# Kernel optimization log

Hardware: AMD Instinct MI355X
Metric: run time of the kernel (lower is better)

The kernel has to match this reference:

```python
import jax, jax.numpy as jnp
import numpy as np

HIDDEN = 2048
N_HEAD = 16
N_KV_HEAD = 4
HEAD_DIM = HIDDEN // N_HEAD
B, S = 2, 2048


def setup_inputs() -> dict:
    key = jax.random.key(0)
    ks = jax.random.split(key, 10)
    scale = 1.0 / np.sqrt(HIDDEN)
    x = jax.random.normal(ks[0], (B, S, HIDDEN), dtype=jnp.float32)
    # causal additive mask, broadcastable over batch and heads
    causal = jnp.tril(jnp.ones((S, S), dtype=jnp.bool_))
    attention_mask = jnp.where(causal, 0.0, -1e9).astype(jnp.float32)[None, None]
    wq_w = jax.random.uniform(ks[1], (HIDDEN, HIDDEN), jnp.float32, -scale, scale)
    wq_b = jax.random.uniform(ks[2], (HIDDEN,), jnp.float32, -scale, scale)
    wk_w = jax.random.uniform(ks[3], (N_KV_HEAD * HEAD_DIM, HIDDEN), jnp.float32, -scale, scale)
    wk_b = jax.random.uniform(ks[4], (N_KV_HEAD * HEAD_DIM,), jnp.float32, -scale, scale)
    wv_w = jax.random.uniform(ks[5], (N_KV_HEAD * HEAD_DIM, HIDDEN), jnp.float32, -scale, scale)
    wv_b = jax.random.uniform(ks[6], (N_KV_HEAD * HEAD_DIM,), jnp.float32, -scale, scale)
    wo_w = jax.random.uniform(ks[7], (HIDDEN, HIDDEN), jnp.float32, -scale, scale)
    wo_b = jax.random.uniform(ks[8], (HIDDEN,), jnp.float32, -scale, scale)
    return dict(x=x, attention_mask=attention_mask, wq_w=wq_w, wq_b=wq_b,
                wk_w=wk_w, wk_b=wk_b, wv_w=wv_w, wv_b=wv_b, wo_w=wo_w, wo_b=wo_b)


def reference(x, attention_mask, wq_w, wq_b, wk_w, wk_b, wv_w, wv_b, wo_w, wo_b):
    bs, seq_len, _ = x.shape
    group = N_HEAD // N_KV_HEAD
    q = x @ wq_w.T + wq_b  # [B,S,H*D]
    k = x @ wk_w.T + wk_b  # [B,S,Hkv*D]
    v = x @ wv_w.T + wv_b
    q = q.reshape(bs, seq_len, N_HEAD, HEAD_DIM).transpose(0, 2, 1, 3)        # [B,H,S,D]
    k = k.reshape(bs, seq_len, N_KV_HEAD, HEAD_DIM).transpose(0, 2, 1, 3)     # [B,Hkv,S,D]
    v = v.reshape(bs, seq_len, N_KV_HEAD, HEAD_DIM).transpose(0, 2, 1, 3)
    # GQA: share each kv head across `group` query heads (repeat_interleave equiv)
    qg = q.reshape(bs, N_KV_HEAD, group, seq_len, HEAD_DIM)
    scores = jnp.einsum('bkgqd,bkld->bkgql', qg, k) / np.sqrt(HEAD_DIM)       # [B,Hkv,g,S,S]
    scores = scores + attention_mask[:, :, None]  # mask broadcast over head dims
    attn = jax.nn.softmax(scores, axis=-1)  # dropout is identity at inference
    out = jnp.einsum('bkgql,bkld->bkgqd', attn, v)                             # [B,Hkv,g,S,D]
    out = out.reshape(bs, N_HEAD, seq_len, HEAD_DIM).transpose(0, 2, 1, 3)
    out = out.reshape(bs, seq_len, HIDDEN)
    return out @ wo_w.T + wo_b
```

## Files before the change

kernel.cpp:

```cpp
#include <hip/hip_runtime.h>

typedef __bf16 bf16;
typedef __bf16 bf16x8 __attribute__((ext_vector_type(8)));
typedef __bf16 bf16x4 __attribute__((ext_vector_type(4)));
typedef __bf16 bf16x2 __attribute__((ext_vector_type(2)));
typedef float  f32x4  __attribute__((ext_vector_type(4)));

#define HIDDEN 2048
#define NH 16
#define NKV 4
#define HD 128
#define BB 2
#define SS 2048
#define MTOT (BB*SS)
#define KVD (NKV*HD)

__device__ __forceinline__ void gload_lds16(const void* g, void* l) {
  __builtin_amdgcn_global_load_lds(
      (__attribute__((address_space(1))) void*)(void*)g,
      (__attribute__((address_space(3))) void*)l,
      16, 0, 0);
}

__global__ void detect_dtype(const unsigned short* __restrict__ x, int* __restrict__ flag) {
  __shared__ int cnt;
  if (threadIdx.x == 0) cnt = 0;
  __syncthreads();
  int c = 0;
  for (int i = threadIdx.x; i < 8192; i += blockDim.x) {
    float v = fabsf(__uint_as_float((unsigned)x[i] << 16));
    if (v > 64.0f || (v > 0.0f && v < 9.5367431640625e-07f)) ++c;
  }
  atomicAdd(&cnt, c);
  __syncthreads();
  if (threadIdx.x == 0) flag[0] = (cnt > 1024) ? 1 : 0;
}

struct ConvJobs {
  const void* src[8];
  bf16*       dst[8];
  long long   n[8];
};

__global__ void conv_multi(ConvJobs jobs, const int* __restrict__ flag) {
  const int f = flag[0];
  const int a = blockIdx.y;
  const long long n = jobs.n[a];
  bf16* dst = jobs.dst[a];
  long long i = (long long)blockIdx.x * blockDim.x + threadIdx.x;
  const long long stride = (long long)gridDim.x * blockDim.x;
  if (f) {
    const float* s = (const float*)jobs.src[a];
    for (; i < n; i += stride) dst[i] = (bf16)s[i];
  } else {
    const bf16* s = (const bf16*)jobs.src[a];
    for (; i < n; i += stride) dst[i] = s[i];
  }
}

__global__ void conv_one(const void* __restrict__ src, bf16* __restrict__ dst,
                         long long n, const int* __restrict__ flag) {
  const int f = flag[0];
  long long i = (long long)blockIdx.x * blockDim.x + threadIdx.x;
  const long long stride = (long long)gridDim.x * blockDim.x;
  if (f) {
    const float* s = (const float*)src;
    for (; i < n; i += stride) dst[i] = (bf16)s[i];
  } else {
    const bf16* s = (const bf16*)src;
    for (; i < n; i += stride) dst[i] = s[i];
  }
}

__global__ __launch_bounds__(256)
void gemm_qkv(const bf16* __restrict__ A,
              const bf16* __restrict__ wq, const bf16* __restrict__ bq,
              const bf16* __restrict__ wk, const bf16* __restrict__ bk,
              const bf16* __restrict__ wv, const bf16* __restrict__ bv,
              bf16* __restrict__ Cq, bf16* __restrict__ Ck, bf16* __restrict__ Cvt)
{
  __shared__ bf16 As[128*32];
  __shared__ bf16 Bs[128*32];
  const int bx = blockIdx.x;
  const bf16 *W, *bias;
  int n0, mode;
  if (bx < 16)      { W = wq; bias = bq; n0 = bx*128;      mode = 0; }
  else if (bx < 20) { W = wk; bias = bk; n0 = (bx-16)*128; mode = 1; }
  else              { W = wv; bias = bv; n0 = (bx-20)*128; mode = 2; }

  const int tid  = threadIdx.x;
  const int wave = tid >> 6, lane = tid & 63;
  const int g = lane >> 4, l15 = lane & 15;
  const int m0 = blockIdx.y * 128;
  const int wm = (wave >> 1) * 64, wn = (wave & 1) * 64;
  const int srow = lane >> 2;
  const int scol = (lane & 3) * 8;
  f32x4 acc[4][4] = {};

  for (int k0 = 0; k0 < HIDDEN; k0 += 32) {
    #pragma unroll
    for (int i = 0; i < 2; ++i) {
      const int seg = wave*2 + i;
      const int row = seg*16 + srow;
      gload_lds16(A + (size_t)(m0+row)*HIDDEN + k0 + scol, &As[row*32 + scol]);
      gload_lds16(W + (size_t)(n0+row)*HIDDEN + k0 + scol, &Bs[row*32 + scol]);
    }
    asm volatile("s_waitcnt vmcnt(0)" ::: "memory");
    __syncthreads();
    bf16x8 af[4], bfr[4];
    #pragma unroll
    for (int m = 0; m < 4; ++m)
      af[m] = *(const bf16x8*)&As[(wm + m*16 + l15)*32 + g*8];
    #pragma unroll
    for (int n = 0; n < 4; ++n)
      bfr[n] = *(const bf16x8*)&Bs[(wn + n*16 + l15)*32 + g*8];
    #pragma unroll
    for (int m = 0; m < 4; ++m)
      #pragma unroll
      for (int n = 0; n < 4; ++n)
        acc[m][n] = __builtin_amdgcn_mfma_f32_16x16x32_bf16(af[m], bfr[n], acc[m][n], 0, 0, 0);
    __syncthreads();
  }
  if (mode == 2) {
    #pragma unroll
    for (int n = 0; n < 4; ++n) {
      const int cc = n0 + wn + n*16 + l15;
      const float bv2 = (float)bias[cc];
      #pragma unroll
      for (int m = 0; m < 4; ++m) {
        const int row = m0 + wm + m*16 + g*4;
        bf16x4 o4;
        #pragma unroll
        for (int r = 0; r < 4; ++r) o4[r] = (bf16)(acc[m][n][r] + bv2);
        *(bf16x4*)&Cvt[(size_t)cc*MTOT + row] = o4;
      }
    }
  } else {
    bf16* Cb = (mode == 0) ? Cq : Ck;
    const int N = (mode == 0) ? HIDDEN : KVD;
    #pragma unroll
    for (int n = 0; n < 4; ++n) {
      const int col = n0 + wn + n*16 + l15;
      const float bv2 = (float)bias[col];
      #pragma unroll
      for (int m = 0; m < 4; ++m) {
        const int row = m0 + wm + m*16 + g*4;
        #pragma unroll
        for (int r = 0; r < 4; ++r)
          Cb[(size_t)(row + r)*N + col] = (bf16)(acc[m][n][r] + bv2);
      }
    }
  }
}

__global__ __launch_bounds__(256)
void gemm_bt(const bf16* __restrict__ A, const bf16* __restrict__ W,
             const bf16* __restrict__ bias, void* __restrict__ C,
             int M, int N, int K, const int* __restrict__ flagp)
{
  __shared__ bf16 As[128*32];
  __shared__ bf16 Bs[128*32];
  const int tid  = threadIdx.x;
  const int wave = tid >> 6, lane = tid & 63;
  const int g = lane >> 4, l15 = lane & 15;
  const int m0 = blockIdx.y * 128, n0 = blockIdx.x * 128;
  const int wm = (wave >> 1) * 64, wn = (wave & 1) * 64;
  const int srow = lane >> 2;
  const int scol = (lane & 3) * 8;
  f32x4 acc[4][4] = {};

  for (int k0 = 0; k0 < K; k0 += 32) {
    #pragma unroll
    for (int i = 0; i < 2; ++i) {
      const int seg = wave*2 + i;
      const int row = seg*16 + srow;
      gload_lds16(A + (size_t)(m0+row)*K + k0 + scol, &As[row*32 + scol]);
      gload_lds16(W + (size_t)(n0+row)*K + k0 + scol, &Bs[row*32 + scol]);
    }
    asm volatile("s_waitcnt vmcnt(0)" ::: "memory");
    __syncthreads();
    bf16x8 af[4], bfr[4];
    #pragma unroll
    for (int m = 0; m < 4; ++m)
      af[m] = *(const bf16x8*)&As[(wm + m*16 + l15)*32 + g*8];
    #pragma unroll
    for (int n = 0; n < 4; ++n)
      bfr[n] = *(const bf16x8*)&Bs[(wn + n*16 + l15)*32 + g*8];
    #pragma unroll
    for (int m = 0; m < 4; ++m)
      #pragma unroll
      for (int n = 0; n < 4; ++n)
        acc[m][n] = __builtin_amdgcn_mfma_f32_16x16x32_bf16(af[m], bfr[n], acc[m][n], 0, 0, 0);
    __syncthreads();
  }
  const int outf = flagp ? flagp[0] : 0;
  if (outf) {
    float* Cf = (float*)C;
    #pragma unroll
    for (int n = 0; n < 4; ++n) {
      const int col = n0 + wn + n*16 + l15;
      const float bv = (float)bias[col];
      #pragma unroll
      for (int m = 0; m < 4; ++m) {
        const int row = m0 + wm + m*16 + g*4;
        #pragma unroll
        for (int r = 0; r < 4; ++r)
          Cf[(size_t)(row + r)*N + col] = acc[m][n][r] + bv;
      }
    }
  } else {
    bf16* Cb = (bf16*)C;
    #pragma unroll
    for (int n = 0; n < 4; ++n) {
      const int col = n0 + wn + n*16 + l15;
      const float bv = (float)bias[col];
      #pragma unroll
      for (int m = 0; m < 4; ++m) {
        const int row = m0 + wm + m*16 + g*4;
        #pragma unroll
        for (int r = 0; r < 4; ++r)
          Cb[(size_t)(row + r)*N + col] = (bf16)(acc[m][n][r] + bv);
      }
    }
  }
}

#define QB 64
#define PPAD 72

__global__ __launch_bounds__(256)
void attn_fwd(const bf16* __restrict__ Q, const bf16* __restrict__ K,
              const bf16* __restrict__ Vt, bf16* __restrict__ O)
{
  __shared__ bf16 Ks[2][64*128];
  __shared__ bf16 Vs[2][128*64];
  __shared__ bf16 Pl[4][16][PPAD];
  const int tid = threadIdx.x, wave = tid >> 6, lane = tid & 63;
  const int g = lane >> 4, l15 = lane & 15;
  const int bh = blockIdx.y;
  const int b = bh >> 4, h = bh & 15, kvh = h >> 2;
  const bf16* Qh = Q + ((size_t)b*SS)*HIDDEN + h*HD;
  const bf16* Kh = K + ((size_t)b*SS)*KVD + kvh*HD;
  const bf16* Vh = Vt + ((size_t)kvh*HD)*MTOT + (size_t)b*SS;
  bf16*       Oh = O + ((size_t)b*SS)*HIDDEN + h*HD;

  const float scale  = 0.08838834764831845f;
  const float L2E    = 1.4426950408889634f;
  const float NEGBIG = -1.0e30f;

  const int krow_st = (lane >> 4);
  const int vrow_st = (lane >> 3);
  const int ksc     = (lane & 15);
  const int vsc     = (lane & 7) ^ (lane >> 3);

  #pragma unroll 1
  for (int pass = 0; pass < 2; ++pass) {
    const int qt = pass ? (31 - (int)blockIdx.x) : (int)blockIdx.x;
    const int qrow0 = qt*QB + wave*16;
    const int qg    = qrow0 + l15;

    bf16x8 bq[4];
    #pragma unroll
    for (int c = 0; c < 4; ++c)
      bq[c] = *(const bf16x8*)(Qh + (size_t)(qrow0 + l15)*HIDDEN + c*32 + g*8);

    f32x4 od[8] = {};
    float m_run = NEGBIG, l_part = 0.f;
    const int ntiles = qt + 1;

    {
      const int kv0 = 0;
      #pragma unroll
      for (int i = 0; i < 4; ++i) {
        const int s = wave*4 + i;
        const int kr = s*4 + krow_st;
        const int kc = ksc ^ (kr & 7);
        gload_lds16(Kh + (size_t)(kv0 + kr)*KVD + kc*8, &Ks[0][s*512 + lane*8]);
        const int vr = s*8 + vrow_st;
        gload_lds16(Vh + (size_t)vr*MTOT + kv0 + vsc*8, &Vs[0][s*512 + lane*8]);
      }
    }
    asm volatile("s_waitcnt vmcnt(0)" ::: "memory");
    __syncthreads();

    int buf = 0;
    #pragma unroll 1
    for (int t = 0; t < ntiles; ++t) {
      const int kv0 = t * 64;

      if (t + 1 < ntiles) {
        const int kv1 = kv0 + 64;
        #pragma unroll
        for (int i = 0; i < 4; ++i) {
          const int s = wave*4 + i;
          const int kr = s*4 + krow_st;
          const int kc = ksc ^ (kr & 7);
          gload_lds16(Kh + (size_t)(kv1 + kr)*KVD + kc*8, &Ks[buf^1][s*512 + lane*8]);
          const int vr = s*8 + vrow_st;
          gload_lds16(Vh + (size_t)vr*MTOT + kv1 + vsc*8, &Vs[buf^1][s*512 + lane*8]);
        }
      }

      f32x4 st[4];
      #pragma unroll
      for (int nb = 0; nb < 4; ++nb) {
        f32x4 s = {};
        #pragma unroll
        for (int c = 0; c < 4; ++c) {
          const int krow = nb*16 + l15;
          const int kch  = (c*4 + g) ^ (krow & 7);
          bf16x8 ka = *(const bf16x8*)&Ks[buf][krow*128 + kch*8];
          s = __builtin_amdgcn_mfma_f32_16x16x32_bf16(ka, bq[c], s, 0, 0, 0);
        }
        st[nb] = s;
      }

      float x[16];
      float mt = NEGBIG;
      #pragma unroll
      for (int nb = 0; nb < 4; ++nb)
        #pragma unroll
        for (int r = 0; r < 4; ++r) {
          const int kv = kv0 + nb*16 + g*4 + r;
          float v = st[nb][r] * scale;
          v = (kv <= qg) ? v : NEGBIG;
          x[nb*4 + r] = v;
          mt = fmaxf(mt, v);
        }
      mt = fmaxf(mt, __shfl_xor(mt, 16, 64));
      mt = fmaxf(mt, __shfl_xor(mt, 32, 64));
      const float m_new = fmaxf(m_run, mt);
      const float corr  = __builtin_amdgcn_exp2f((m_run - m_new) * L2E);

      float psum = 0.f;
      bf16x2 pk[4][2];
      #pragma unroll
      for (int nb = 0; nb < 4; ++nb) {
        const float p0 = __builtin_amdgcn_exp2f((x[nb*4+0] - m_new) * L2E);
        const float p1 = __builtin_amdgcn_exp2f((x[nb*4+1] - m_new) * L2E);
        const float p2 = __builtin_amdgcn_exp2f((x[nb*4+2] - m_new) * L2E);
        const float p3 = __builtin_amdgcn_exp2f((x[nb*4+3] - m_new) * L2E);
        psum += p0 + p1 + p2 + p3;
        pk[nb][0] = bf16x2{(bf16)p0, (bf16)p1};
        pk[nb][1] = bf16x2{(bf16)p2, (bf16)p3};
      }
      l_part = l_part * corr + psum;
      m_run  = m_new;
      #pragma unroll
      for (int db = 0; db < 8; ++db) od[db] *= corr;

      #pragma unroll
      for (int nb = 0; nb < 4; ++nb) {
        *(bf16x2*)&Pl[wave][l15][nb*16 + g*4 + 0] = pk[nb][0];
        *(bf16x2*)&Pl[wave][l15][nb*16 + g*4 + 2] = pk[nb][1];
      }
      asm volatile("s_waitcnt lgkmcnt(0)" ::: "memory");
      __builtin_amdgcn_sched_barrier(0);

      #pragma unroll
      for (int c = 0; c < 2; ++c) {
        bf16x8 pb = *(const bf16x8*)&Pl[wave][l15][c*32 + g*8];
        #pragma unroll
        for (int db = 0; db < 8; ++db) {
          const int vrow = db*16 + l15;
          const int vch  = (c*4 + g) ^ (l15 & 7);
          bf16x8 va = *(const bf16x8*)&Vs[buf][vrow*64 + vch*8];
          od[db] = __builtin_amdgcn_mfma_f32_16x16x32_bf16(va, pb, od[db], 0, 0, 0);
        }
      }

      asm volatile("s_waitcnt vmcnt(0)" ::: "memory");
      __syncthreads();
      buf ^= 1;
    }

    float lt = l_part;
    lt += __shfl_xor(lt, 16, 64);
    lt += __shfl_xor(lt, 32, 64);
    const float inv = 1.0f / lt;
    #pragma unroll
    for (int db = 0; db < 8; ++db) {
      bf16x4 o4;
      #pragma unroll
      for (int r = 0; r < 4; ++r) o4[r] = (bf16)(od[db][r] * inv);
      *(bf16x4*)(Oh + (size_t)qg*HIDDEN + db*16 + g*4) = o4;
    }
  }
}

extern "C" void kernel_launch(void* const* d_in, const int* in_sizes, int n_in,
                              void* d_out, int out_size, void* d_ws, size_t ws_size,
                              hipStream_t stream)
{
  (void)in_sizes; (void)n_in; (void)out_size; (void)ws_size;
  const void* x    = d_in[0];
  const void* wq_w = d_in[2];
  const void* wq_b = d_in[3];
  const void* wk_w = d_in[4];
  const void* wk_b = d_in[5];
  const void* wv_w = d_in[6];
  const void* wv_b = d_in[7];
  const void* wo_w = d_in[8];
  const void* wo_b = d_in[9];

  int*  flag = (int*)d_ws;
  bf16* base = (bf16*)((char*)d_ws + 256);
  const long long NX  = (long long)MTOT*HIDDEN;
  const long long NWQ = (long long)HIDDEN*HIDDEN;
  const long long NWK = (long long)KVD*HIDDEN;
  bf16* x_ao = base;
  bf16* wqwo = x_ao + NX;
  bf16* wk_c = wqwo + NWQ;
  bf16* wv_c = wk_c + NWK;
  bf16* bq_c = wv_c + NWK;
  bf16* bk_c = bq_c + 2048;
  bf16* bv_c = bk_c + 512;
  bf16* bo_c = bv_c + 512;
  bf16* q_ws  = bo_c + 2048;
  bf16* k_ws  = q_ws + NX;
  bf16* vt_ws = k_ws + (long long)MTOT*KVD;

  detect_dtype<<<1, 256, 0, stream>>>((const unsigned short*)x, flag);

  ConvJobs jb;
  jb.src[0] = x;    jb.dst[0] = x_ao; jb.n[0] = NX;
  jb.src[1] = wq_w; jb.dst[1] = wqwo; jb.n[1] = NWQ;
  jb.src[2] = wk_w; jb.dst[2] = wk_c; jb.n[2] = NWK;
  jb.src[3] = wv_w; jb.dst[3] = wv_c; jb.n[3] = NWK;
  jb.src[4] = wq_b; jb.dst[4] = bq_c; jb.n[4] = 2048;
  jb.src[5] = wk_b; jb.dst[5] = bk_c; jb.n[5] = 512;
  jb.src[6] = wv_b; jb.dst[6] = bv_c; jb.n[6] = 512;
  jb.src[7] = wo_b; jb.dst[7] = bo_c; jb.n[7] = 2048;
  conv_multi<<<dim3(1024, 8), 256, 0, stream>>>(jb, flag);

  gemm_qkv<<<dim3(24, MTOT/128), 256, 0, stream>>>(x_ao, wqwo, bq_c, wk_c, bk_c,
                                                   wv_c, bv_c, q_ws, k_ws, vt_ws);

  conv_one<<<dim3(1024), 256, 0, stream>>>(wo_w, wqwo, NWQ, flag);

  attn_fwd<<<dim3(16, BB*NH), 256, 0, stream>>>(q_ws, k_ws, vt_ws, x_ao);

  gemm_bt<<<dim3(HIDDEN/128, MTOT/128), 256, 0, stream>>>(x_ao, wqwo, bo_c, d_out, MTOT, HIDDEN, HIDDEN, flag);
}
```

Measured before the change: 250.0 us.

## Triple-buffer LDS tiles in QKV and output GEMMs to overlap loads with MFMA

Both GEMM kernels now keep three LDS buffers per operand and prefetch the tile two steps ahead with global_load_lds, while the current tile is computed. The per-step vmcnt(0) wait plus two __syncthreads become a single partial wait vmcnt(4) and one scheduling-fenced barrier. This hides global load latency behind MFMA work, at the cost of triple the LDS footprint (48KB per block), which may lower occupancy. Correctness depends on the vmcnt count matching four outstanding loads per stage, and the single barrier must also protect the buffer being overwritten next.

```diff
diff --git a/kernel.cpp b/kernel.cpp
--- a/kernel.cpp
+++ b/kernel.cpp
@@ -72,6 +72,12 @@
   }
 }
 
+__device__ __forceinline__ void pipe_barrier() {
+  __builtin_amdgcn_sched_barrier(0);
+  __builtin_amdgcn_s_barrier();
+  __builtin_amdgcn_sched_barrier(0);
+}
+
 __global__ __launch_bounds__(256)
 void gemm_qkv(const bf16* __restrict__ A,
               const bf16* __restrict__ wq, const bf16* __restrict__ bq,
@@ -79,8 +85,8 @@
               const bf16* __restrict__ wv, const bf16* __restrict__ bv,
               bf16* __restrict__ Cq, bf16* __restrict__ Ck, bf16* __restrict__ Cvt)
 {
-  __shared__ bf16 As[128*32];
-  __shared__ bf16 Bs[128*32];
+  __shared__ bf16 As[3][128*32];
+  __shared__ bf16 Bs[3][128*32];
   const int bx = blockIdx.x;
   const bf16 *W, *bias;
   int n0, mode;
@@ -97,30 +103,49 @@
   const int scol = (lane & 3) * 8;
   f32x4 acc[4][4] = {};
 
-  for (int k0 = 0; k0 < HIDDEN; k0 += 32) {
+  auto stage = [&](int bi, int k0) {
     #pragma unroll
     for (int i = 0; i < 2; ++i) {
       const int seg = wave*2 + i;
       const int row = seg*16 + srow;
-      gload_lds16(A + (size_t)(m0+row)*HIDDEN + k0 + scol, &As[row*32 + scol]);
-      gload_lds16(W + (size_t)(n0+row)*HIDDEN + k0 + scol, &Bs[row*32 + scol]);
-    }
-    asm volatile("s_waitcnt vmcnt(0)" ::: "memory");
-    __syncthreads();
+      gload_lds16(A + (size_t)(m0+row)*HIDDEN + k0 + scol, &As[bi][row*32 + scol]);
+      gload_lds16(W + (size_t)(n0+row)*HIDDEN + k0 + scol, &Bs[bi][row*32 + scol]);
+    }
+  };
+  auto compute = [&](int bi) {
     bf16x8 af[4], bfr[4];
     #pragma unroll
     for (int m = 0; m < 4; ++m)
-      af[m] = *(const bf16x8*)&As[(wm + m*16 + l15)*32 + g*8];
+      af[m] = *(const bf16x8*)&As[bi][(wm + m*16 + l15)*32 + g*8];
     #pragma unroll
     for (int n = 0; n < 4; ++n)
-      bfr[n] = *(const bf16x8*)&Bs[(wn + n*16 + l15)*32 + g*8];
+      bfr[n] = *(const bf16x8*)&Bs[bi][(wn + n*16 + l15)*32 + g*8];
     #pragma unroll
     for (int m = 0; m < 4; ++m)
       #pragma unroll
       for (int n = 0; n < 4; ++n)
         acc[m][n] = __builtin_amdgcn_mfma_f32_16x16x32_bf16(af[m], bfr[n], acc[m][n], 0, 0, 0);
-    __syncthreads();
-  }
+  };
+
+  const int nt = HIDDEN / 32;
+  stage(0, 0);
+  stage(1, 32);
+  asm volatile("s_waitcnt vmcnt(4)" ::: "memory");
+  pipe_barrier();
+
+  int c0 = 0, c1 = 1, c2 = 2;
+  for (int t = 0; t < nt - 2; ++t) {
+    stage(c2, (t + 2) * 32);
+    compute(c0);
+    asm volatile("s_waitcnt vmcnt(4)" ::: "memory");
+    pipe_barrier();
+    const int tmp = c0; c0 = c1; c1 = c2; c2 = tmp;
+  }
+  compute(c0);
+  asm volatile("s_waitcnt vmcnt(0)" ::: "memory");
+  pipe_barrier();
+  compute(c1);
+
   if (mode == 2) {
     #pragma unroll
     for (int n = 0; n < 4; ++n) {
@@ -158,8 +183,8 @@
              const bf16* __restrict__ bias, void* __restrict__ C,
              int M, int N, int K, const int* __restrict__ flagp)
 {
-  __shared__ bf16 As[128*32];
-  __shared__ bf16 Bs[128*32];
+  __shared__ bf16 As[3][128*32];
+  __shared__ bf16 Bs[3][128*32];
   const int tid  = threadIdx.x;
   const int wave = tid >> 6, lane = tid & 63;
   const int g = lane >> 4, l15 = lane & 15;
@@ -169,30 +194,49 @@
   const int scol = (lane & 3) * 8;
   f32x4 acc[4][4] = {};
 
-  for (int k0 = 0; k0 < K; k0 += 32) {
+  auto stage = [&](int bi, int k0) {
     #pragma unroll
     for (int i = 0; i < 2; ++i) {
       const int seg = wave*2 + i;
       const int row = seg*16 + srow;
-      gload_lds16(A + (size_t)(m0+row)*K + k0 + scol, &As[row*32 + scol]);
-      gload_lds16(W + (size_t)(n0+row)*K + k0 + scol, &Bs[row*32 + scol]);
-    }
-    asm volatile("s_waitcnt vmcnt(0)" ::: "memory");
-    __syncthreads();
+      gload_lds16(A + (size_t)(m0+row)*K + k0 + scol, &As[bi][row*32 + scol]);
+      gload_lds16(W + (size_t)(n0+row)*K + k0 + scol, &Bs[bi][row*32 + scol]);
+    }
+  };
+  auto compute = [&](int bi) {
     bf16x8 af[4], bfr[4];
     #pragma unroll
     for (int m = 0; m < 4; ++m)
-      af[m] = *(const bf16x8*)&As[(wm + m*16 + l15)*32 + g*8];
+      af[m] = *(const bf16x8*)&As[bi][(wm + m*16 + l15)*32 + g*8];
     #pragma unroll
     for (int n = 0; n < 4; ++n)
-      bfr[n] = *(const bf16x8*)&Bs[(wn + n*16 + l15)*32 + g*8];
+      bfr[n] = *(const bf16x8*)&Bs[bi][(wn + n*16 + l15)*32 + g*8];
     #pragma unroll
     for (int m = 0; m < 4; ++m)
       #pragma unroll
       for (int n = 0; n < 4; ++n)
         acc[m][n] = __builtin_amdgcn_mfma_f32_16x16x32_bf16(af[m], bfr[n], acc[m][n], 0, 0, 0);
-    __syncthreads();
-  }
+  };
+
+  const int nt = K / 32;
+  stage(0, 0);
+  stage(1, 32);
+  asm volatile("s_waitcnt vmcnt(4)" ::: "memory");
+  pipe_barrier();
+
+  int c0 = 0, c1 = 1, c2 = 2;
+  for (int t = 0; t < nt - 2; ++t) {
+    stage(c2, (t + 2) * 32);
+    compute(c0);
+    asm volatile("s_waitcnt vmcnt(4)" ::: "memory");
+    pipe_barrier();
+    const int tmp = c0; c0 = c1; c1 = c2; c2 = tmp;
+  }
+  compute(c0);
+  asm volatile("s_waitcnt vmcnt(0)" ::: "memory");
+  pipe_barrier();
+  compute(c1);
+
   const int outf = flagp ? flagp[0] : 0;
   if (outf) {
     float* Cf = (float*)C;
```

New measurement: 254.0 us. No clear change (+1.6%).
